# Kernel optimization log

Hardware: AMD Instinct MI355X
Metric: run time of the kernel (lower is better)

Reference implementation:

```python
import jax, jax.numpy as jnp
import numpy as np

# --- config (matches init_kwargs) ---
HID = 2048      # hidden_size
H = 16          # num_attention_heads
D_NOPE = 128    # qk_nope_head_dim
D_ROPE = 64     # qk_rope_head_dim
D_Q = D_NOPE + D_ROPE  # 192
D_V = 128       # v_head_dim
QR = 1536       # q_lora_rank
KVR = 512       # kv_lora_rank
PH = 16         # pattern_heads
PD = HID // PH  # 128
THETA = 10000.0
EPS = 1e-6


def rmsnorm(x, w):
    var = jnp.mean(jnp.square(x), axis=-1, keepdims=True)
    return x * jax.lax.rsqrt(var + EPS) * w


def rope_cos_sin(seq_len):
    inv_freq = 1.0 / (THETA ** (jnp.arange(0, D_ROPE, 2, dtype=jnp.float32) / D_ROPE))
    t = jnp.arange(seq_len, dtype=jnp.float32)
    freqs = jnp.outer(t, inv_freq)            # [S, D_ROPE/2]
    emb = jnp.concatenate([freqs, freqs], -1)  # [S, D_ROPE]
    return jnp.cos(emb), jnp.sin(emb)


def rotate_half(x):
    x1, x2 = jnp.split(x, 2, axis=-1)
    return jnp.concatenate([-x2, x1], axis=-1)


def apply_rope(x, cos, sin):
    # x: [B, H, S, D_ROPE]; cos/sin: [S, D_ROPE]
    return x * cos[None, None] + rotate_half(x) * sin[None, None]


def setup_inputs() -> dict:
    key = jax.random.key(0)
    ks = jax.random.split(key, 12)
    def w(k, shape):
        return (jax.random.normal(k, shape, jnp.float32) / np.sqrt(shape[-1])).astype(jnp.float32)
    B, S = 2, 1024
    return {
        "hidden_states": jax.random.normal(ks[0], (B, S, HID), jnp.float32),
        "q_a_w": w(ks[1], (QR, HID)),
        "q_a_ln_w": jnp.ones((QR,), jnp.float32),
        "q_b_w": w(ks[2], (H * D_Q, QR)),
        "kv_a_w": w(ks[3], (KVR + H * D_ROPE, HID)),
        "kv_a_ln_w": jnp.ones((KVR,), jnp.float32),
        "kv_b_w": w(ks[4], (H * (D_NOPE + D_V), KVR)),
        "o_w": w(ks[5], (HID, H * D_V)),
        "sp_q_w": w(ks[6], (HID, HID)),
        "sp_k_w": w(ks[7], (HID, HID)),
        "sp_v_w": w(ks[8], (HID, HID)),
        "sp_o_w": w(ks[9], (HID, HID)),
        "gate_w": w(ks[10], (2, HID)),
        "gate_b": jnp.zeros((2,), jnp.float32),
    }


def reference(hidden_states, q_a_w, q_a_ln_w, q_b_w, kv_a_w, kv_a_ln_w, kv_b_w,
              o_w, sp_q_w, sp_k_w, sp_v_w, sp_o_w, gate_w, gate_b):
    b, s, _ = hidden_states.shape
    dt = hidden_states.dtype

    # ---- main MLA path ----
    q_mid = rmsnorm(hidden_states @ q_a_w.T, q_a_ln_w)                      # [B,S,QR]
    q = (q_mid @ q_b_w.T).reshape(b, s, H, D_Q).transpose(0, 2, 1, 3)       # [B,H,S,Dq]
    q_nope, q_pe = q[..., :D_NOPE], q[..., D_NOPE:]

    kv_a = hidden_states @ kv_a_w.T                                         # [B,S,KVR+H*Dr]
    kv_lora, k_pe_flat = kv_a[..., :KVR], kv_a[..., KVR:]
    k_pe = k_pe_flat.reshape(b, s, H, D_ROPE).transpose(0, 2, 1, 3)         # [B,H,S,Dr]

    kv = (rmsnorm(kv_lora, kv_a_ln_w) @ kv_b_w.T)
    kv = kv.reshape(b, s, H, D_NOPE + D_V).transpose(0, 2, 1, 3)            # [B,H,S,Dn+Dv]
    k_nope, v = kv[..., :D_NOPE], kv[..., D_NOPE:]

    cos, sin = rope_cos_sin(s)
    q_pe = apply_rope(q_pe, cos, sin)
    k_pe = apply_rope(k_pe, cos, sin)

    qf = jnp.concatenate([q_nope, q_pe], -1)                                # [B,H,S,Dq]
    kf = jnp.concatenate([k_nope, k_pe], -1)

    scale = D_Q ** -0.5
    scores = jnp.einsum('bhqd,bhkd->bhqk', qf, kf) * scale
    probs = jax.nn.softmax(scores.astype(jnp.float32), axis=-1).astype(dt)
    ctx = jnp.einsum('bhqk,bhkd->bhqd', probs, v)                           # [B,H,S,Dv]
    main_out = ctx.transpose(0, 2, 1, 3).reshape(b, s, H * D_V) @ o_w.T     # [B,S,HID]

    # ---- self pattern path (standard MHA on hidden_states) ----
    def split_heads(x):
        return x.reshape(b, s, PH, PD).transpose(0, 2, 1, 3)
    pq = split_heads(hidden_states @ sp_q_w.T)
    pk = split_heads(hidden_states @ sp_k_w.T)
    pv = split_heads(hidden_states @ sp_v_w.T)
    p_scores = jnp.einsum('bhqd,bhkd->bhqk', pq, pk) * (PD ** -0.5)
    p_probs = jax.nn.softmax(p_scores.astype(jnp.float32), axis=-1).astype(dt)
    p_ctx = jnp.einsum('bhqk,bhkd->bhqd', p_probs, pv)
    pattern_out = p_ctx.transpose(0, 2, 1, 3).reshape(b, s, HID) @ sp_o_w.T

    # ---- learned gate over paths ----
    gates = jax.nn.softmax(hidden_states @ gate_w.T + gate_b, axis=-1)      # [B,S,2]
    return gates[..., 0:1] * main_out + gates[..., 1:2] * pattern_out
```

## Files before the change

kernel.cpp:

```cpp
#include <hip/hip_runtime.h>
#include <math.h>
#include <stdint.h>

#define HIDN  2048
#define NH    16
#define DNOPE 128
#define DROPE 64
#define DQ    192
#define DV    128
#define QRANK 1536
#define KVRANK 512
#define SEQ   1024
#define NBATCH 2
#define NTOK  (NBATCH*SEQ)
#define EPSV  1e-6f

typedef unsigned short u16;
typedef unsigned int   u32;
typedef __attribute__((ext_vector_type(8))) short  short8;
typedef __attribute__((ext_vector_type(8))) unsigned short ushort8;
typedef __attribute__((ext_vector_type(4))) float  f32x4;

__device__ __forceinline__ u16 f2b(float f) {
    u32 u = __float_as_uint(f);
    u = (u + 0x7fffu + ((u >> 16) & 1u)) >> 16;
    return (u16)u;
}
__device__ __forceinline__ float b2f(u16 h) {
    return __uint_as_float(((u32)h) << 16);
}

__device__ __forceinline__ void async_copy16(const u16* g, u16* l) {
    __builtin_amdgcn_global_load_lds(
        (const __attribute__((address_space(1))) u32*)g,
        (__attribute__((address_space(3))) u32*)l,
        16, 0, 0);
}

__device__ __forceinline__ int swz(int r, int c) { return r * 4 + (c ^ ((r >> 1) & 3)); }

#define DPP_ROR(x, ctrl) __int_as_float(__builtin_amdgcn_update_dpp( \
    __float_as_int(x), __float_as_int(x), ctrl, 0xF, 0xF, false))

__device__ __forceinline__ float rowmax16(float x) {
    x = fmaxf(x, DPP_ROR(x, 0x121));
    x = fmaxf(x, DPP_ROR(x, 0x122));
    x = fmaxf(x, DPP_ROR(x, 0x124));
    x = fmaxf(x, DPP_ROR(x, 0x128));
    return x;
}
__device__ __forceinline__ float rowsum16(float x) {
    x += DPP_ROR(x, 0x121);
    x += DPP_ROR(x, 0x122);
    x += DPP_ROR(x, 0x124);
    x += DPP_ROR(x, 0x128);
    return x;
}

struct CastArgs {
    const float* s[10];
    u16* d[10];
    int cum[11];
    const float* lnq;
    const float* lnkv;
};
__global__ __launch_bounds__(256)
void cast_all(CastArgs a, int total_chunks)
{
    int c = blockIdx.x * 256 + threadIdx.x;
    if (c >= total_chunks) return;
    int seg = 0;
    #pragma unroll
    for (int i = 1; i < 10; ++i) seg += (c >= a.cum[i]) ? 1 : 0;
    int local = c - a.cum[seg];
    const float* src = a.s[seg] + (size_t)local * 8;
    u16* dst = a.d[seg] + (size_t)local * 8;
    float4 x = *(const float4*)(src);
    float4 y = *(const float4*)(src + 4);
    if (seg == 3 || seg == 4) {
        const float* ln = (seg == 3) ? a.lnq : a.lnkv;
        u32 kmod = (seg == 3) ? (u32)QRANK : (u32)KVRANK;
        u32 kb = ((u32)local * 8u) % kmod;
        float4 w0 = *(const float4*)(ln + kb);
        float4 w1 = *(const float4*)(ln + kb + 4);
        x.x *= w0.x; x.y *= w0.y; x.z *= w0.z; x.w *= w0.w;
        y.x *= w1.x; y.y *= w1.y; y.z *= w1.z; y.w *= w1.w;
    }
    ushort8 o;
    o[0]=f2b(x.x); o[1]=f2b(x.y); o[2]=f2b(x.z); o[3]=f2b(x.w);
    o[4]=f2b(y.x); o[5]=f2b(y.y); o[6]=f2b(y.z); o[7]=f2b(y.w);
    *(ushort8*)(dst) = o;
}

struct GemmSeg {
    const u16* X; const u16* W;
    float* Cf; u16* Cb; u16* Cb2; u16* Cb3;
    int K; int ldx; int ldc; int mode; int bx0;
};
struct GemmArgs { GemmSeg seg[3]; int nseg; float* ssq; float* sskv; };

__global__ __launch_bounds__(256)
void gemm_multi(GemmArgs a)
{
    __shared__ __align__(16) u16 As[2 * 4096];
    __shared__ __align__(16) u16 Bs[2 * 4096];
    int s = 0;
    if (a.nseg > 1 && (int)blockIdx.y >= a.seg[1].bx0) s = 1;
    if (a.nseg > 2 && (int)blockIdx.y >= a.seg[2].bx0) s = 2;
    const GemmSeg g = a.seg[s];

    const int tid = threadIdx.x;
    const int bn = ((int)blockIdx.y - g.bx0) * 128;
    const int bm = blockIdx.x * 128;
    const int lane = tid & 63, wv = tid >> 6;
    const int lm = lane & 15, lq = lane >> 4;
    const int wm = (wv >> 1) * 64, wn = (wv & 1) * 64;
    const int ldx = g.ldx, K = g.K;
    const u16* Xp = g.X;
    const u16* Wp = g.W;

    auto stage = [&](int kt, int buf) {
        int k0 = kt * 32;
        #pragma unroll
        for (int it = 0; it < 2; ++it) {
            int base = wv * 64 + it * 256;
            int slot = base + lane;
            int r = slot >> 2, c = (slot & 3) ^ ((r >> 1) & 3);
            async_copy16(Xp + (size_t)(bm + r) * ldx + k0 + c * 8,
                         As + buf * 4096 + base * 8);
            async_copy16(Wp + (size_t)(bn + r) * K + k0 + c * 8,
                         Bs + buf * 4096 + base * 8);
        }
    };

    f32x4 acc[4][4] = {};
    const int niter = K >> 5;
    stage(0, 0);
    for (int kt = 0; kt < niter; ++kt) {
        int cur = kt & 1;
        __syncthreads();
        if (kt + 1 < niter) stage(kt + 1, cur ^ 1);
        const u16* Ab = As + cur * 4096;
        const u16* Bb = Bs + cur * 4096;
        short8 af[4], bf[4];
        #pragma unroll
        for (int mt = 0; mt < 4; ++mt) {
            int R = wm + mt * 16 + lm;
            af[mt] = *(const short8*)(Ab + swz(R, lq) * 8);
        }
        #pragma unroll
        for (int nt = 0; nt < 4; ++nt) {
            int R = wn + nt * 16 + lm;
            bf[nt] = *(const short8*)(Bb + swz(R, lq) * 8);
        }
        #pragma unroll
        for (int mt = 0; mt < 4; ++mt)
            #pragma unroll
            for (int nt = 0; nt < 4; ++nt)
                acc[mt][nt] = __builtin_amdgcn_mfma_f32_16x16x32_bf16(
                    af[mt], bf[nt], acc[mt][nt], 0, 0, 0);
    }

    const int mode = g.mode;
    if (mode == 1) {
        const int h2  = (bn + wn) / DQ;
        const int hd0 = (bn + wn) % DQ;
        const bool ropeH = (hd0 == 128);
        float invf0 = 0.f, invf1 = 0.f;
        if (ropeH) {
            invf0 = exp2f((float)lm * -0.41524101186f);
            invf1 = exp2f((float)(16 + lm) * -0.41524101186f);
        }
        #pragma unroll
        for (int mt = 0; mt < 4; ++mt) {
            int token0 = bm + wm + mt * 16 + lq * 4;
            #pragma unroll
            for (int i = 0; i < 4; ++i) {
                int tok = token0 + i;
                int b2 = tok >> 10, s2 = tok & (SEQ - 1);
                float inv = rsqrtf(a.ssq[tok] * (1.f / QRANK) + EPSV);
                u16* row = g.Cb + ((size_t)((b2 * NH + h2) * SEQ + s2)) * DQ + hd0;
                if (!ropeH) {
                    #pragma unroll
                    for (int nt = 0; nt < 4; ++nt)
                        row[nt * 16 + lm] = f2b(acc[mt][nt][i] * inv);
                } else {
                    float sn0, c0, sn1, c1;
                    sincosf((float)s2 * invf0, &sn0, &c0);
                    sincosf((float)s2 * invf1, &sn1, &c1);
                    float x10 = acc[mt][0][i] * inv, x20 = acc[mt][2][i] * inv;
                    float x11 = acc[mt][1][i] * inv, x21 = acc[mt][3][i] * inv;
                    row[lm]          = f2b(x10 * c0 - x20 * sn0);
                    row[32 + lm]     = f2b(x20 * c0 + x10 * sn0);
                    row[16 + lm]     = f2b(x11 * c1 - x21 * sn1);
                    row[48 + lm]     = f2b(x21 * c1 + x11 * sn1);
                }
            }
        }
        return;
    }
    #pragma unroll
    for (int mt = 0; mt < 4; ++mt) {
        int token0 = bm + wm + mt * 16 + lq * 4;
        #pragma unroll
        for (int i = 0; i < 4; ++i) {
            int tok = token0 + i;
            int b2 = tok >> 10, s2 = tok & (SEQ - 1);
            float invkv = 1.f;
            if (mode == 3) invkv = rsqrtf(a.sskv[tok] * (1.f / KVRANK) + EPSV);
            #pragma unroll
            for (int nt = 0; nt < 4; ++nt) {
                int feat = bn + wn + nt * 16 + lm;
                float v = acc[mt][nt][i];
                if (mode == 0) {
                    g.Cf[(size_t)tok * g.ldc + feat] = v;
                } else if (mode == 5) {
                    g.Cb[(size_t)tok * g.ldc + feat] = f2b(v);
                } else if (mode == 3) {
                    v *= invkv;
                    int h2 = feat >> 8, c = feat & 255;
                    if (c < 128)
                        g.Cb[((size_t)((b2 * NH + h2) * SEQ + s2)) * DQ + c] = f2b(v);
                    else
                        g.Cb2[((size_t)((b2 * NH + h2) * 128 + (c - 128))) * SEQ + s2] = f2b(v);
                } else {
                    int wsel = feat >> 11;
                    int f2 = feat & 2047;
                    int h2 = f2 >> 7, d = f2 & 127;
                    if (wsel == 0)
                        g.Cb[((size_t)((b2 * NH + h2) * SEQ + s2)) * 128 + d] = f2b(v);
                    else if (wsel == 1)
                        g.Cb2[((size_t)((b2 * NH + h2) * SEQ + s2)) * 128 + d] = f2b(v);
                    else
                        g.Cb3[((size_t)((b2 * NH + h2) * 128 + d)) * SEQ + s2] = f2b(v);
                }
            }
        }
    }
    if (mode == 5) {
        float* ssp = nullptr;
        if (bn < QRANK) ssp = a.ssq;
        else if (bn < QRANK + KVRANK) ssp = a.sskv;
        if (ssp) {
            #pragma unroll
            for (int mt = 0; mt < 4; ++mt) {
                int token0 = bm + wm + mt * 16 + lq * 4;
                #pragma unroll
                for (int i = 0; i < 4; ++i) {
                    float sq = 0.f;
                    #pragma unroll
                    for (int nt = 0; nt < 4; ++nt) {
                        float v = acc[mt][nt][i];
                        sq += v * v;
                    }
                    sq = rowsum16(sq);
                    if (lm == 0) atomicAdd(&ssp[token0 + i], sq);
                }
            }
        }
    }
}

__global__ __launch_bounds__(256)
void rope_k(const u16* __restrict__ amid, u16* __restrict__ kf)
{
    int t = blockIdx.x * 256 + threadIdx.x;
    int i = t & 31, s = (t >> 5) & (SEQ - 1), bh = t >> 15;
    float inv_freq = exp2f((float)i * -0.41524101186f);
    float ang = (float)s * inv_freq;
    float c, sn; sincosf(ang, &sn, &c);
    int h = bh & (NH - 1), bb = bh >> 4;
    const u16* src = amid + ((size_t)(bb * SEQ + s)) * 3072 + (QRANK + KVRANK) + h * DROPE;
    float x1 = b2f(src[i]), x2 = b2f(src[32 + i]);
    u16* dst = kf + ((size_t)bh * SEQ + s) * DQ + DNOPE;
    dst[i]      = f2b(x1 * c - x2 * sn);
    dst[32 + i] = f2b(x2 * c + x1 * sn);
}

template<int DQK>
__device__ __forceinline__
void flash_body(const u16* __restrict__ Q, const u16* __restrict__ Kf,
                const u16* __restrict__ Vt, u16* __restrict__ ctx_out,
                float scale, u16* Ks, u16* Vs, u16* Ps, int qt, int h, int bb)
{
    constexpr int KSZ  = 32 * DQK;
    constexpr int VSZ  = 32 * 128;
    constexpr int NKIT = DQK / 64;
    constexpr int NT   = SEQ / 32;
    const int tid = threadIdx.x, lane = tid & 63, wv = tid >> 6;
    const int lm = lane & 15, lq = lane >> 4;
    const size_t bh = (size_t)bb * NH + h;
    const u16* Qb = Q + (bh * SEQ + qt * 128 + wv * 32) * (size_t)DQK;
    const u16* Kb = Kf + bh * SEQ * (size_t)DQK;
    const u16* Vb = Vt + bh * (size_t)128 * SEQ;

    short8 qfrag[2][DQK / 32];
    #pragma unroll
    for (int rh = 0; rh < 2; ++rh)
        #pragma unroll
        for (int ks = 0; ks < DQK / 32; ++ks)
            qfrag[rh][ks] = *(const short8*)(Qb + (rh * 16 + lm) * DQK + ks * 32 + lq * 8);

    auto stage = [&](int kt, int buf) {
        #pragma unroll
        for (int it = 0; it < NKIT; ++it) {
            int base = it * 256 + wv * 64;
            int slot = base + lane;
            int plane = slot >> 7, rem = slot & 127;
            int key = rem >> 2, c = (rem & 3) ^ ((key >> 1) & 3);
            async_copy16(Kb + (size_t)(kt * 32 + key) * DQK + plane * 32 + c * 8,
                         Ks + buf * KSZ + base * 8);
        }
        #pragma unroll
        for (int it = 0; it < 2; ++it) {
            int base = it * 256 + wv * 64;
            int slot = base + lane;
            int d = slot >> 2, c = (slot & 3) ^ ((d >> 1) & 3);
            async_copy16(Vb + (size_t)d * SEQ + kt * 32 + c * 8,
                         Vs + buf * VSZ + base * 8);
        }
    };

    float m_i[2][4], l_i[2][4];
    #pragma unroll
    for (int rh = 0; rh < 2; ++rh)
        #pragma unroll
        for (int i = 0; i < 4; ++i) { m_i[rh][i] = -INFINITY; l_i[rh][i] = 0.f; }
    f32x4 oacc[2][8] = {};

    stage(0, 0);
    for (int kt = 0; kt < NT; ++kt) {
        int cur = kt & 1;
        __syncthreads();
        if (kt + 1 < NT) stage(kt + 1, cur ^ 1);
        const u16* Kc = Ks + cur * KSZ;
        const u16* Vc = Vs + cur * VSZ;

        f32x4 sacc[2][2] = {};
        #pragma unroll
        for (int kb = 0; kb < 2; ++kb)
            #pragma unroll
            for (int ks = 0; ks < DQK / 32; ++ks) {
                int R = kb * 16 + lm;
                short8 kfr = *(const short8*)(Kc + ks * 1024 + swz(R, lq) * 8);
                sacc[0][kb] = __builtin_amdgcn_mfma_f32_16x16x32_bf16(
                    qfrag[0][ks], kfr, sacc[0][kb], 0, 0, 0);
                sacc[1][kb] = __builtin_amdgcn_mfma_f32_16x16x32_bf16(
                    qfrag[1][ks], kfr, sacc[1][kb], 0, 0, 0);
            }

        float p0[2][4], p1[2][4], mx[2][4];
        bool needb = false;
        #pragma unroll
        for (int rh = 0; rh < 2; ++rh)
            #pragma unroll
            for (int i = 0; i < 4; ++i) {
                float s0 = sacc[rh][0][i] * scale, s1 = sacc[rh][1][i] * scale;
                float m2 = rowmax16(fmaxf(s0, s1));
                p0[rh][i] = s0; p1[rh][i] = s1; mx[rh][i] = m2;
                needb |= (m2 > m_i[rh][i] + 8.f);
            }
        bool need = __any(needb);
        float alpha[2][4];
        if (need) {
            #pragma unroll
            for (int rh = 0; rh < 2; ++rh)
                #pragma unroll
                for (int i = 0; i < 4; ++i) {
                    float mnew = fmaxf(m_i[rh][i], mx[rh][i]);
                    alpha[rh][i] = __expf(m_i[rh][i] - mnew);
                    m_i[rh][i] = mnew;
                    l_i[rh][i] *= alpha[rh][i];
                }
        }
        #pragma unroll
        for (int rh = 0; rh < 2; ++rh)
            #pragma unroll
            for (int i = 0; i < 4; ++i) {
                p0[rh][i] = __expf(p0[rh][i] - m_i[rh][i]);
                p1[rh][i] = __expf(p1[rh][i] - m_i[rh][i]);
                l_i[rh][i] += rowsum16(p0[rh][i] + p1[rh][i]);
            }

        u16* Pw = Ps + wv * 1280;
        #pragma unroll
        for (int rh = 0; rh < 2; ++rh)
            #pragma unroll
            for (int i = 0; i < 4; ++i) {
                Pw[(rh * 16 + lq * 4 + i) * 40 + lm]      = f2b(p0[rh][i]);
                Pw[(rh * 16 + lq * 4 + i) * 40 + 16 + lm] = f2b(p1[rh][i]);
            }
        short8 pfrag0 = *(const short8*)(Pw + lm * 40 + lq * 8);
        short8 pfrag1 = *(const short8*)(Pw + (16 + lm) * 40 + lq * 8);

        if (need) {
            #pragma unroll
            for (int rh = 0; rh < 2; ++rh)
                #pragma unroll
                for (int nt = 0; nt < 8; ++nt)
                    #pragma unroll
                    for (int i = 0; i < 4; ++i) oacc[rh][nt][i] *= alpha[rh][i];
        }
        #pragma unroll
        for (int nt = 0; nt < 8; ++nt) {
            int R = nt * 16 + lm;
            short8 vfr = *(const short8*)(Vc + swz(R, lq) * 8);
            oacc[0][nt] = __builtin_amdgcn_mfma_f32_16x16x32_bf16(
                pfrag0, vfr, oacc[0][nt], 0, 0, 0);
            oacc[1][nt] = __builtin_amdgcn_mfma_f32_16x16x32_bf16(
                pfrag1, vfr, oacc[1][nt], 0, 0, 0);
        }
    }

    #pragma unroll
    for (int rh = 0; rh < 2; ++rh) {
        int s0 = qt * 128 + wv * 32 + rh * 16 + lq * 4;
        #pragma unroll
        for (int i = 0; i < 4; ++i) {
            float inv = 1.f / l_i[rh][i];
            u16* dst = ctx_out + ((size_t)(bb * SEQ + s0 + i) * NH + h) * 128;
            #pragma unroll
            for (int nt = 0; nt < 8; ++nt)
                dst[nt * 16 + lm] = f2b(oacc[rh][nt][i] * inv);
        }
    }
}

__global__ __launch_bounds__(256, 2)
void flash_fused(const u16* qf, const u16* kf, const u16* Vtg, u16* ctx,
                 const u16* pq, const u16* pk, const u16* pvt, u16* p_ctx,
                 float scale_main, float scale_pat)
{
    __shared__ __align__(16) u16 Ks[2 * 32 * DQ];
    __shared__ __align__(16) u16 Vs[2 * 32 * 128];
    __shared__ __align__(16) u16 Ps[4 * 32 * 40];
    int h = blockIdx.x, qtb = blockIdx.y, bb = blockIdx.z;
    if (qtb < 8)
        flash_body<DQ>(qf, kf, Vtg, ctx, scale_main, Ks, Vs, Ps, qtb, h, bb);
    else
        flash_body<128>(pq, pk, pvt, p_ctx, scale_pat, Ks, Vs, Ps, qtb - 8, h, bb);
}

__global__ __launch_bounds__(256)
void gate_combine(const float* __restrict__ x, const float* __restrict__ gw,
                  const float* __restrict__ gb,
                  const float* __restrict__ mo, const float* __restrict__ po,
                  float* __restrict__ out)
{
    const int tok = blockIdx.x;
    const float* xr = x + (size_t)tok * HIDN;
    float d0 = 0.f, d1 = 0.f;
    for (int i = threadIdx.x; i < HIDN; i += 256) {
        float v = xr[i];
        d0 += v * gw[i];
        d1 += v * gw[HIDN + i];
    }
    __shared__ float r0[256], r1[256];
    r0[threadIdx.x] = d0; r1[threadIdx.x] = d1;
    __syncthreads();
    for (int off = 128; off > 0; off >>= 1) {
        if (threadIdx.x < off) {
            r0[threadIdx.x] += r0[threadIdx.x + off];
            r1[threadIdx.x] += r1[threadIdx.x + off];
        }
        __syncthreads();
    }
    float l0 = r0[0] + gb[0], l1 = r1[0] + gb[1];
    float m = fmaxf(l0, l1);
    float e0 = __expf(l0 - m), e1 = __expf(l1 - m);
    float g0 = e0 / (e0 + e1), g1 = e1 / (e0 + e1);
    const float* mr = mo + (size_t)tok * HIDN;
    const float* pr = po + (size_t)tok * HIDN;
    float* orow = out + (size_t)tok * HIDN;
    for (int i = threadIdx.x; i < HIDN; i += 256)
        orow[i] = g0 * mr[i] + g1 * pr[i];
}

extern "C" void kernel_launch(void* const* d_in, const int* in_sizes, int n_in,
                              void* d_out, int out_size, void* d_ws, size_t ws_size,
                              hipStream_t stream)
{
    const float* X        = (const float*)d_in[0];
    const float* q_a_w    = (const float*)d_in[1];
    const float* q_a_ln_w = (const float*)d_in[2];
    const float* q_b_w    = (const float*)d_in[3];
    const float* kv_a_w   = (const float*)d_in[4];
    const float* kv_a_ln_w= (const float*)d_in[5];
    const float* kv_b_w   = (const float*)d_in[6];
    const float* o_w      = (const float*)d_in[7];
    const float* sp_q_w   = (const float*)d_in[8];
    const float* sp_k_w   = (const float*)d_in[9];
    const float* sp_v_w   = (const float*)d_in[10];
    const float* sp_o_w   = (const float*)d_in[11];
    const float* gate_w   = (const float*)d_in[12];
    const float* gate_b   = (const float*)d_in[13];
    float* out = (float*)d_out;

    char* p = (char*)d_ws;
    auto alloc = [&](size_t bytes) -> char* {
        char* r = p; p += (bytes + 255) & ~(size_t)255; return r;
    };
    u16* amid      = (u16*)alloc((size_t)NTOK * 3072 * 2);
    u16* Xb        = (u16*)alloc((size_t)NTOK * HIDN * 2);
    u16* aw_b      = (u16*)alloc((size_t)3072 * HIDN * 2);
    u16* q_b_wb    = (u16*)alloc((size_t)NH * DQ * QRANK * 2);
    u16* kv_b_wb   = (u16*)alloc((size_t)NH * 256 * KVRANK * 2);
    u16* o_wb      = (u16*)alloc((size_t)HIDN * HIDN * 2);
    u16* spqkv_wb  = (u16*)alloc((size_t)3 * HIDN * HIDN * 2);
    u16* sp_o_wb   = (u16*)alloc((size_t)HIDN * HIDN * 2);
    u16* qf        = (u16*)alloc((size_t)NTOK * NH * DQ * 2);
    u16* kf        = (u16*)alloc((size_t)NTOK * NH * DQ * 2);
    u16* Vtg       = (u16*)alloc((size_t)NBATCH * NH * 128 * SEQ * 2);
    u16* pq        = (u16*)alloc((size_t)NTOK * HIDN * 2);
    u16* pk        = (u16*)alloc((size_t)NTOK * HIDN * 2);
    float* ssbuf   = (float*)alloc((size_t)2 * NTOK * 4);
    u16* pvt    = aw_b;
    u16* ctx    = q_b_wb;
    u16* p_ctx  = spqkv_wb;
    float* patout = (float*)qf;
    float* ss_q  = ssbuf;
    float* ss_kv = ssbuf + NTOK;

    dim3 blk(256);

    hipMemsetAsync(ssbuf, 0, (size_t)2 * NTOK * 4, stream);

    CastArgs ca;
    const float* srcs[10] = {X, q_a_w, kv_a_w, q_b_w, kv_b_w, o_w,
                             sp_q_w, sp_k_w, sp_v_w, sp_o_w};
    u16* dsts[10] = {Xb, aw_b, aw_b + (size_t)QRANK * HIDN, q_b_wb, kv_b_wb, o_wb,
                     spqkv_wb, spqkv_wb + (size_t)HIDN * HIDN,
                     spqkv_wb + (size_t)2 * HIDN * HIDN, sp_o_wb};
    int ns[10] = {NTOK * HIDN, QRANK * HIDN, 1536 * HIDN, NH * DQ * QRANK,
                  NH * 256 * KVRANK, HIDN * HIDN, HIDN * HIDN, HIDN * HIDN,
                  HIDN * HIDN, HIDN * HIDN};
    int cum = 0;
    for (int i = 0; i < 10; ++i) {
        ca.s[i] = srcs[i]; ca.d[i] = dsts[i];
        ca.cum[i] = cum; cum += ns[i] / 8;
    }
    ca.cum[10] = cum;
    ca.lnq = q_a_ln_w; ca.lnkv = kv_a_ln_w;
    cast_all<<<dim3((cum + 255) / 256), blk, 0, stream>>>(ca, cum);

    {
        GemmArgs ga = {};
        ga.nseg = 1;
        ga.seg[0] = {Xb, aw_b, nullptr, amid, nullptr, nullptr,
                     HIDN, HIDN, 3072, 5, 0};
        ga.ssq = ss_q; ga.sskv = ss_kv;
        gemm_multi<<<dim3(16, 24), blk, 0, stream>>>(ga);
    }

    {
        GemmArgs ga = {};
        ga.nseg = 3;
        ga.seg[0] = {Xb, spqkv_wb, nullptr, pq, pk, pvt,
                     HIDN, HIDN, 0, 4, 0};
        ga.seg[1] = {amid, q_b_wb, nullptr, qf, nullptr, nullptr,
                     QRANK, 3072, 0, 1, 48};
        ga.seg[2] = {amid + QRANK, kv_b_wb, nullptr, kf, Vtg, nullptr,
                     KVRANK, 3072, 0, 3, 72};
        ga.ssq = ss_q; ga.sskv = ss_kv;
        gemm_multi<<<dim3(16, 104), blk, 0, stream>>>(ga);
    }

    rope_k<<<dim3(4096), blk, 0, stream>>>(amid, kf);

    flash_fused<<<dim3(NH, 16, NBATCH), blk, 0, stream>>>(
        qf, kf, Vtg, ctx, pq, pk, pvt, p_ctx,
        1.0f / sqrtf((float)DQ), 1.0f / sqrtf(128.0f));

    {
        GemmArgs ga = {};
        ga.nseg = 2;
        ga.seg[0] = {ctx, o_wb, out, nullptr, nullptr, nullptr,
                     HIDN, HIDN, HIDN, 0, 0};
        ga.seg[1] = {p_ctx, sp_o_wb, patout, nullptr, nullptr, nullptr,
                     HIDN, HIDN, HIDN, 0, 16};
        gemm_multi<<<dim3(16, 32), blk, 0, stream>>>(ga);
    }

    gate_combine<<<dim3(NTOK), blk, 0, stream>>>(X, gate_w, gate_b, out, patout, out);
}
```

Measured before the change: 529.4 us.

## Fuse both output projections and gated combine into one GEMM epilogue

Replaces the two-segment output-projection GEMM plus the separate gate_combine pass with a single kernel. Each block accumulates both ctx@o_w and p_ctx@sp_o_w for the same output tile and writes the gate-weighted sum directly. Gates are computed earlier by a small standalone kernel. This removes the fp32 round trip of two full [2048x2048] intermediates, but halves the grid to 256 blocks, each doing twice the K work, which lowers parallelism.

```diff
diff --git a/kernel.cpp b/kernel.cpp
--- a/kernel.cpp
+++ b/kernel.cpp
@@ -262,6 +262,112 @@
 }
 
 __global__ __launch_bounds__(256)
+void gemm_oproj(const u16* __restrict__ ctxp, const u16* __restrict__ ow,
+                const u16* __restrict__ pctxp, const u16* __restrict__ spw,
+                const float2* __restrict__ gates, float* __restrict__ out)
+{
+    __shared__ __align__(16) u16 As[2 * 4096];
+    __shared__ __align__(16) u16 Bs[2 * 4096];
+    const int tid = threadIdx.x;
+    const int bn = blockIdx.y * 128;
+    const int bm = blockIdx.x * 128;
+    const int lane = tid & 63, wv = tid >> 6;
+    const int lm = lane & 15, lq = lane >> 4;
+    const int wm = (wv >> 1) * 64, wn = (wv & 1) * 64;
+
+    f32x4 acc0[4][4] = {};
+    f32x4 acc1[4][4] = {};
+
+    auto kloop = [&](const u16* Xp, const u16* Wp, f32x4 (&acc)[4][4]) {
+        auto stage = [&](int kt, int buf) {
+            int k0 = kt * 32;
+            #pragma unroll
+            for (int it = 0; it < 2; ++it) {
+                int base = wv * 64 + it * 256;
+                int slot = base + lane;
+                int r = slot >> 2, c = (slot & 3) ^ ((r >> 1) & 3);
+                async_copy16(Xp + (size_t)(bm + r) * HIDN + k0 + c * 8,
+                             As + buf * 4096 + base * 8);
+                async_copy16(Wp + (size_t)(bn + r) * HIDN + k0 + c * 8,
+                             Bs + buf * 4096 + base * 8);
+            }
+        };
+        const int niter = HIDN >> 5;
+        stage(0, 0);
+        for (int kt = 0; kt < niter; ++kt) {
+            int cur = kt & 1;
+            __syncthreads();
+            if (kt + 1 < niter) stage(kt + 1, cur ^ 1);
+            const u16* Ab = As + cur * 4096;
+            const u16* Bb = Bs + cur * 4096;
+            short8 af[4], bf[4];
+            #pragma unroll
+            for (int mt = 0; mt < 4; ++mt)
+                af[mt] = *(const short8*)(Ab + swz(wm + mt * 16 + lm, lq) * 8);
+            #pragma unroll
+            for (int nt = 0; nt < 4; ++nt)
+                bf[nt] = *(const short8*)(Bb + swz(wn + nt * 16 + lm, lq) * 8);
+            #pragma unroll
+            for (int mt = 0; mt < 4; ++mt)
+                #pragma unroll
+                for (int nt = 0; nt < 4; ++nt)
+                    acc[mt][nt] = __builtin_amdgcn_mfma_f32_16x16x32_bf16(
+                        af[mt], bf[nt], acc[mt][nt], 0, 0, 0);
+        }
+    };
+
+    kloop(ctxp,  ow,  acc0);
+    kloop(pctxp, spw, acc1);
+
+    #pragma unroll
+    for (int mt = 0; mt < 4; ++mt) {
+        int token0 = bm + wm + mt * 16 + lq * 4;
+        #pragma unroll
+        for (int i = 0; i < 4; ++i) {
+            int tok = token0 + i;
+            float2 gv = gates[tok];
+            float* orow = out + (size_t)tok * HIDN;
+            #pragma unroll
+            for (int nt = 0; nt < 4; ++nt) {
+                int feat = bn + wn + nt * 16 + lm;
+                orow[feat] = gv.x * acc0[mt][nt][i] + gv.y * acc1[mt][nt][i];
+            }
+        }
+    }
+}
+
+__global__ __launch_bounds__(256)
+void gate_kern(const float* __restrict__ x, const float* __restrict__ gw,
+               const float* __restrict__ gb, float2* __restrict__ gates)
+{
+    const int tok = blockIdx.x;
+    const float* xr = x + (size_t)tok * HIDN;
+    float d0 = 0.f, d1 = 0.f;
+    for (int i = threadIdx.x; i < HIDN; i += 256) {
+        float v = xr[i];
+        d0 += v * gw[i];
+        d1 += v * gw[HIDN + i];
+    }
+    __shared__ float r0[256], r1[256];
+    r0[threadIdx.x] = d0; r1[threadIdx.x] = d1;
+    __syncthreads();
+    for (int off = 128; off > 0; off >>= 1) {
+        if (threadIdx.x < off) {
+            r0[threadIdx.x] += r0[threadIdx.x + off];
+            r1[threadIdx.x] += r1[threadIdx.x + off];
+        }
+        __syncthreads();
+    }
+    if (threadIdx.x == 0) {
+        float l0 = r0[0] + gb[0], l1 = r1[0] + gb[1];
+        float m = fmaxf(l0, l1);
+        float e0 = __expf(l0 - m), e1 = __expf(l1 - m);
+        float inv = 1.f / (e0 + e1);
+        gates[tok] = make_float2(e0 * inv, e1 * inv);
+    }
+}
+
+__global__ __launch_bounds__(256)
 void rope_k(const u16* __restrict__ amid, u16* __restrict__ kf)
 {
     int t = blockIdx.x * 256 + threadIdx.x;
@@ -439,41 +545,6 @@
         flash_body<DQ>(qf, kf, Vtg, ctx, scale_main, Ks, Vs, Ps, qtb, h, bb);
     else
         flash_body<128>(pq, pk, pvt, p_ctx, scale_pat, Ks, Vs, Ps, qtb - 8, h, bb);
-}
-
-__global__ __launch_bounds__(256)
-void gate_combine(const float* __restrict__ x, const float* __restrict__ gw,
-                  const float* __restrict__ gb,
-                  const float* __restrict__ mo, const float* __restrict__ po,
-                  float* __restrict__ out)
-{
-    const int tok = blockIdx.x;
-    const float* xr = x + (size_t)tok * HIDN;
-    float d0 = 0.f, d1 = 0.f;
-    for (int i = threadIdx.x; i < HIDN; i += 256) {
-        float v = xr[i];
-        d0 += v * gw[i];
-        d1 += v * gw[HIDN + i];
-    }
-    __shared__ float r0[256], r1[256];
-    r0[threadIdx.x] = d0; r1[threadIdx.x] = d1;
-    __syncthreads();
-    for (int off = 128; off > 0; off >>= 1) {
-        if (threadIdx.x < off) {
-            r0[threadIdx.x] += r0[threadIdx.x + off];
-            r1[threadIdx.x] += r1[threadIdx.x + off];
-        }
-        __syncthreads();
-    }
-    float l0 = r0[0] + gb[0], l1 = r1[0] + gb[1];
-    float m = fmaxf(l0, l1);
-    float e0 = __expf(l0 - m), e1 = __expf(l1 - m);
-    float g0 = e0 / (e0 + e1), g1 = e1 / (e0 + e1);
-    const float* mr = mo + (size_t)tok * HIDN;
-    const float* pr = po + (size_t)tok * HIDN;
-    float* orow = out + (size_t)tok * HIDN;
-    for (int i = threadIdx.x; i < HIDN; i += 256)
-        orow[i] = g0 * mr[i] + g1 * pr[i];
 }
 
 extern "C" void kernel_launch(void* const* d_in, const int* in_sizes, int n_in,
@@ -514,10 +585,10 @@
     u16* pq        = (u16*)alloc((size_t)NTOK * HIDN * 2);
     u16* pk        = (u16*)alloc((size_t)NTOK * HIDN * 2);
     float* ssbuf   = (float*)alloc((size_t)2 * NTOK * 4);
+    float2* gates  = (float2*)alloc((size_t)NTOK * 8);
     u16* pvt    = aw_b;
     u16* ctx    = q_b_wb;
     u16* p_ctx  = spqkv_wb;
-    float* patout = (float*)qf;
     float* ss_q  = ssbuf;
     float* ss_kv = ssbuf + NTOK;
 
@@ -543,6 +614,8 @@
     ca.lnq = q_a_ln_w; ca.lnkv = kv_a_ln_w;
     cast_all<<<dim3((cum + 255) / 256), blk, 0, stream>>>(ca, cum);
 
+    gate_kern<<<dim3(NTOK), blk, 0, stream>>>(X, gate_w, gate_b, gates);
+
     {
         GemmArgs ga = {};
         ga.nseg = 1;
@@ -571,15 +644,6 @@
         qf, kf, Vtg, ctx, pq, pk, pvt, p_ctx,
         1.0f / sqrtf((float)DQ), 1.0f / sqrtf(128.0f));
 
-    {
-        GemmArgs ga = {};
-        ga.nseg = 2;
-        ga.seg[0] = {ctx, o_wb, out, nullptr, nullptr, nullptr,
-                     HIDN, HIDN, HIDN, 0, 0};
-        ga.seg[1] = {p_ctx, sp_o_wb, patout, nullptr, nullptr, nullptr,
-                     HIDN, HIDN, HIDN, 0, 16};
-        gemm_multi<<<dim3(16, 32), blk, 0, stream>>>(ga);
-    }
-
-    gate_combine<<<dim3(NTOK), blk, 0, stream>>>(X, gate_w, gate_b, out, patout, out);
-}
+    gemm_oproj<<<dim3(16, 16), blk, 0, stream>>>(
+        ctx, o_wb, p_ctx, sp_o_wb, gates, out);
+}
```

Result: slower. 557.8 us (+5.4%).
